# Kernel tuning notes

Measured on AMD Instinct MI355X. Metric: run time of the kernel, lower is better.

The kernel has to match this reference:

```python
import jax, jax.numpy as jnp
import numpy as np

N_QUBITS = 8
DEPTH = 2
INPUT_DIM = 64
HIDDEN_DIM = 8
SEQ_LEN = 128
BATCH = 512
DIM = 2 ** N_QUBITS


def _build_perm():
    """Compose the depth*n CNOT ring (CNOT(i,(i+1)%n) for i in range(n), repeated DEPTH times)
    into a single basis-state permutation. Wire 0 is the most-significant qubit (torchquantum order).
    CNOT is an involution on basis states: new[s] = old[f(s)], f flips target bit iff control bit set.
    Sequential composition: perm <- perm[f_j]."""
    n = N_QUBITS
    perm = np.arange(DIM)
    for _ in range(DEPTH):
        for c in range(n):
            t = (c + 1) % n
            s = np.arange(DIM)
            cbit = (s >> (n - 1 - c)) & 1
            fs = np.where(cbit == 1, s ^ (1 << (n - 1 - t)), s)
            perm = perm[fs]
    return jnp.asarray(perm, dtype=jnp.int32)


def _build_signs():
    s = np.arange(DIM)[:, None]
    w = np.arange(N_QUBITS)[None, :]
    bits = (s >> (N_QUBITS - 1 - w)) & 1
    return jnp.asarray(1.0 - 2.0 * bits, dtype=jnp.float32)  # [DIM, n]


PERM = _build_perm()
SIGNS = _build_signs()


def _qlayer(ang):
    """QLayer: RX(ang_i) on wire i of |0...0> (encoder RX + trainable RX fused since RX(a)RX(b)=RX(a+b)),
    then DEPTH CNOT-ring layers (precomputed permutation), then PauliZ expectation per wire.
    ang: [B, n] -> returns [B, n]."""
    half = 0.5 * ang
    v0 = jnp.cos(half).astype(jnp.complex64)          # [B, n]
    v1 = (-1j) * jnp.sin(half).astype(jnp.complex64)  # RX|0> = cos(t/2)|0> - i sin(t/2)|1>
    vecs = jnp.stack([v0, v1], axis=-1)               # [B, n, 2]
    b = ang.shape[0]
    state = jnp.ones((b, 1), jnp.complex64)
    for w in range(N_QUBITS):  # build product state, wire 0 most significant
        state = (state[:, :, None] * vecs[:, w, None, :]).reshape(b, -1)
    state = state[:, PERM]  # apply composed CNOT entanglers
    probs = jnp.real(state * jnp.conj(state)).astype(jnp.float32)  # [B, 2^n]
    return probs @ SIGNS  # [B, n] PauliZ expectations


def setup_inputs() -> dict:
    key = jax.random.key(0)
    ks = jax.random.split(key, 14)
    d = {"inputs": jax.random.normal(ks[0], (SEQ_LEN, BATCH, INPUT_DIM), jnp.float32)}
    fan_in = INPUT_DIM + HIDDEN_DIM
    scale = 1.0 / np.sqrt(fan_in)
    names = ["f", "i", "u", "o"]
    for j, nm in enumerate(names):
        d[f"W_{nm}"] = jax.random.uniform(ks[1 + 3 * j], (N_QUBITS, fan_in), jnp.float32, -scale, scale)
        d[f"b_{nm}"] = jax.random.uniform(ks[2 + 3 * j], (N_QUBITS,), jnp.float32, -scale, scale)
        d[f"th_{nm}"] = jax.random.normal(ks[3 + 3 * j], (N_QUBITS,), jnp.float32) * 0.1
    return d


def reference(inputs, W_f, b_f, W_i, b_i, W_u, b_u, W_o, b_o, th_f, th_i, th_u, th_o):
    batch = inputs.shape[1]

    def step(carry, x):
        hx, cx = carry
        comb = jnp.concatenate([x, hx], axis=1)  # [B, input+hidden]
        f = jax.nn.sigmoid(_qlayer(comb @ W_f.T + b_f + th_f))
        i = jax.nn.sigmoid(_qlayer(comb @ W_i.T + b_i + th_i))
        g = jnp.tanh(_qlayer(comb @ W_u.T + b_u + th_u))
        o = jax.nn.sigmoid(_qlayer(comb @ W_o.T + b_o + th_o))
        cx = f * cx + i * g
        hx = o * jnp.tanh(cx)
        return (hx, cx), hx

    init = (jnp.zeros((batch, HIDDEN_DIM), jnp.float32), jnp.zeros((batch, HIDDEN_DIM), jnp.float32))
    (hx, cx), outputs = jax.lax.scan(step, init, inputs)
    return (outputs, (hx, cx))
```

## Files before the change

### kernel.cpp

```cpp
#include <hip/hip_runtime.h>
#include <cstdint>
#include <cstddef>


constexpr int SEQ    = 128;
constexpr int NBATCH = 512;
constexpr int INDIM  = 64;
constexpr int FANIN  = 72;
constexpr long OUT_HX = (long)SEQ * NBATCH * 8;
constexpr long OUT_CX = OUT_HX + (long)NBATCH * 8;

#define SWZ(v, imm) __int_as_float(__builtin_amdgcn_ds_swizzle(__float_as_int(v), (imm)))

__device__ __forceinline__ float fast_cos(float ang) {
    const float rev = ang * 0.15915494309189535f;
    return __builtin_amdgcn_cosf(__builtin_amdgcn_fractf(rev));
}

template <int CTRL> __device__ __forceinline__ float DPPF(float x) {
    return __int_as_float(__builtin_amdgcn_update_dpp(
        0, __float_as_int(x), CTRL, 0xF, 0xF, false));
}

__device__ __forceinline__ float xlane32(float x, bool hiHalf) {
#if __has_builtin(__builtin_amdgcn_permlane32_swap)
    typedef unsigned uint2v __attribute__((ext_vector_type(2)));
    uint2v r = __builtin_amdgcn_permlane32_swap(
        __float_as_uint(x), __float_as_uint(x), false, false);
    return __uint_as_float(hiHalf ? r[0] : r[1]);
#else
    (void)hiHalf;
    return __shfl_xor(x, 32, 64);
#endif
}

__global__ __launch_bounds__(256) void xproj_kernel(
    const float* __restrict__ x,
    const float* __restrict__ Wf, const float* __restrict__ bf, const float* __restrict__ thf,
    const float* __restrict__ Wi, const float* __restrict__ bi, const float* __restrict__ thi,
    const float* __restrict__ Wu, const float* __restrict__ bu, const float* __restrict__ thu,
    const float* __restrict__ Wo, const float* __restrict__ bo, const float* __restrict__ tho,
    float* __restrict__ xp)
{
    __shared__ float lx[128 * 68];
    __shared__ float lbias[32];
    const int tid = threadIdx.x;
    const long rowBase = (long)blockIdx.x * 128;

    if (tid < 32) {
        const int g = tid >> 3, w = tid & 7;
        const float* bg = (g == 0) ? bf : (g == 1) ? bi : (g == 2) ? bu : bo;
        const float* tg = (g == 0) ? thf : (g == 1) ? thi : (g == 2) ? thu : tho;
        lbias[tid] = bg[w] + tg[w];
    }

    const float4* xin = reinterpret_cast<const float4*>(x + rowBase * INDIM);
#pragma unroll
    for (int i = 0; i < 8; ++i) {
        const int f   = i * 256 + tid;
        const int row = f >> 4;
        const int kq  = f & 15;
        *reinterpret_cast<float4*>(&lx[row * 68 + kq * 4]) = xin[f];
    }
    __syncthreads();

    const int og = tid & 3;
    const int q  = tid >> 2;
    const float* Wg = (og == 0) ? Wf : (og == 1) ? Wi : (og == 2) ? Wu : Wo;

    float acc[2][8];
#pragma unroll
    for (int r = 0; r < 2; ++r)
#pragma unroll
        for (int j = 0; j < 8; ++j) acc[r][j] = 0.f;

#pragma unroll
    for (int k4 = 0; k4 < 16; ++k4) {
        const float4 x0 = *reinterpret_cast<const float4*>(&lx[q * 68 + k4 * 4]);
        const float4 x1 = *reinterpret_cast<const float4*>(&lx[(q + 64) * 68 + k4 * 4]);
#pragma unroll
        for (int j = 0; j < 8; ++j) {
            const float4 wv = *reinterpret_cast<const float4*>(Wg + j * FANIN + k4 * 4);
            acc[0][j] = fmaf(x0.x, wv.x, acc[0][j]);
            acc[0][j] = fmaf(x0.y, wv.y, acc[0][j]);
            acc[0][j] = fmaf(x0.z, wv.z, acc[0][j]);
            acc[0][j] = fmaf(x0.w, wv.w, acc[0][j]);
            acc[1][j] = fmaf(x1.x, wv.x, acc[1][j]);
            acc[1][j] = fmaf(x1.y, wv.y, acc[1][j]);
            acc[1][j] = fmaf(x1.z, wv.z, acc[1][j]);
            acc[1][j] = fmaf(x1.w, wv.w, acc[1][j]);
        }
    }

#pragma unroll
    for (int r = 0; r < 2; ++r) {
        float4 o0, o1;
        o0.x = acc[r][0] + lbias[og * 8 + 0];
        o0.y = acc[r][1] + lbias[og * 8 + 1];
        o0.z = acc[r][2] + lbias[og * 8 + 2];
        o0.w = acc[r][3] + lbias[og * 8 + 3];
        o1.x = acc[r][4] + lbias[og * 8 + 4];
        o1.y = acc[r][5] + lbias[og * 8 + 5];
        o1.z = acc[r][6] + lbias[og * 8 + 6];
        o1.w = acc[r][7] + lbias[og * 8 + 7];
        float* dst = xp + (rowBase + q + 64 * r) * 32 + og * 8;
        reinterpret_cast<float4*>(dst)[0] = o0;
        reinterpret_cast<float4*>(dst)[1] = o1;
    }
}

__global__ __launch_bounds__(256) void qlstm_scan_kernel(
    const float* __restrict__ xp,
    const float* __restrict__ Wf, const float* __restrict__ Wi,
    const float* __restrict__ Wu, const float* __restrict__ Wo,
    float* __restrict__ out)
{
    const int tid  = threadIdx.x;
    const int lane = tid & 63;
    const int wv   = tid >> 6;
    const int g1   = (lane >> 5) & 1;
    const int g    = (lane & 1) | (g1 << 1);
    const int w    = (lane >> 1) & 7;
    const int rsub = (lane >> 4) & 1;
    const int row  = (blockIdx.x << 3) + (wv << 1) + rsub;

    const float* Wg = (g == 0) ? Wf : (g == 1) ? Wi : (g == 2) ? Wu : Wo;

    float whx[8];
#pragma unroll
    for (int d = 0; d < 8; ++d) whx[d] = Wg[w * FANIN + 64 + (w ^ d)];

    const unsigned mask = (unsigned)((0x55AAD5EAF5FAFDABull >> (w * 8)) & 0xFFull);
    bool pm[8];
#pragma unroll
    for (int d = 0; d < 8; ++d) pm[d] = ((mask >> (w ^ d)) & 1u) != 0u;

    const bool  isU   = (g == 2);
    const float ZL    = isU ? -2.0f : -1.0f;
    const float A     = isU ?  2.0f :  1.0f;
    const float B     = isU ? -1.0f :  0.0f;
    const bool  gOdd  = (lane & 1) != 0;
    const bool  gHi   = g1 != 0;
    const bool  doOut = (lane & 0x21) == 0;

    const int col = g * 8 + w;

    float hh0=0.f,hh1=0.f,hh2=0.f,hh3=0.f,hh4=0.f,hh5=0.f,hh6=0.f,hh7=0.f;
    float cxl = 0.f;

#define QSTEP(XV, T) do {                                                      \
    const float d0_ = fmaf(hh0, whx[0], fmaf(hh1, whx[1], fmaf(hh2, whx[2], hh3 * whx[3]))); \
    const float d1_ = fmaf(hh4, whx[4], fmaf(hh5, whx[5], fmaf(hh6, whx[6], hh7 * whx[7]))); \
    const float ang_ = (XV) + d0_ + d1_;                                       \
    const float c0_ = fast_cos(ang_);                                          \
    const float c1_ = DPPF<0x4E>(c0_);                                         \
    const float c2_ = DPPF<0x141>(DPPF<0x1B>(c0_));                            \
    const float c3_ = DPPF<0x141>(DPPF<0xB1>(c0_));                            \
    const float c4_ = DPPF<0x128>(c0_);                                        \
    const float c5_ = DPPF<0x128>(DPPF<0x4E>(c0_));                            \
    const float c6_ = DPPF<0x140>(DPPF<0x1B>(c0_));                            \
    const float c7_ = DPPF<0x140>(DPPF<0xB1>(c0_));                            \
    const float z_ = (((pm[0]?c0_:1.0f)*(pm[1]?c1_:1.0f))                      \
                    * ((pm[2]?c2_:1.0f)*(pm[3]?c3_:1.0f)))                     \
                   * (((pm[4]?c4_:1.0f)*(pm[5]?c5_:1.0f))                      \
                    * ((pm[6]?c6_:1.0f)*(pm[7]?c7_:1.0f)));                    \
    const float e_   = __expf(z_ * ZL);                                        \
    const float act_ = fmaf(A, __builtin_amdgcn_rcpf(1.0f + e_), B);           \
    const float a01_ = DPPF<0xB1>(act_);                                       \
    const float ae_  = gOdd ? a01_ : act_;                                     \
    const float ao_  = gOdd ? act_ : a01_;                                     \
    const float be_  = xlane32(ae_, gHi);                                      \
    const float bo_  = xlane32(ao_, gHi);                                      \
    const float fg_  = gHi ? be_ : ae_;                                        \
    const float ig_  = gHi ? bo_ : ao_;                                        \
    const float ug_  = gHi ? ae_ : be_;                                        \
    const float og_  = gHi ? ao_ : bo_;                                        \
    const float ncx_ = fmaf(fg_, cxl, ig_ * ug_);                              \
    const float et_  = __expf(-2.0f * ncx_);                                   \
    const float tc_  = fmaf(2.0f, __builtin_amdgcn_rcpf(1.0f + et_), -1.0f);   \
    const float nhx_ = og_ * tc_;                                              \
    cxl = ncx_;                                                                \
    if (doOut) out[((long)(T) * NBATCH + row) * 8 + w] = nhx_;                 \
    hh0 = nhx_;                                                                \
    hh1 = DPPF<0x4E>(nhx_);                                                    \
    hh2 = DPPF<0x141>(DPPF<0x1B>(nhx_));                                       \
    hh3 = DPPF<0x141>(DPPF<0xB1>(nhx_));                                       \
    hh4 = DPPF<0x128>(nhx_);                                                   \
    hh5 = DPPF<0x128>(DPPF<0x4E>(nhx_));                                       \
    hh6 = DPPF<0x140>(DPPF<0x1B>(nhx_));                                       \
    hh7 = DPPF<0x140>(DPPF<0xB1>(nhx_));                                       \
} while (0)

    float xva[16], xvb[16];
#pragma unroll
    for (int j = 0; j < 16; ++j)
        xva[j] = xp[((long)j * NBATCH + row) * 32 + col];

#pragma unroll 1
    for (int ck = 0; ck < 8; ++ck) {
        const int t0 = ck * 16;
        if (ck < 7) {
#pragma unroll
            for (int j = 0; j < 16; ++j)
                xvb[j] = xp[((long)(t0 + 16 + j) * NBATCH + row) * 32 + col];
        }
#pragma unroll
        for (int j = 0; j < 16; ++j) {
            QSTEP(xva[j], t0 + j);
        }
#pragma unroll
        for (int j = 0; j < 16; ++j) xva[j] = xvb[j];
    }
#undef QSTEP

    if (doOut) {
        out[OUT_HX + (long)row * 8 + w] = hh0;
        out[OUT_CX + (long)row * 8 + w] = cxl;
    }
}

__global__ __launch_bounds__(256) void qlstm_scan_fused(
    const float* __restrict__ x,
    const float* __restrict__ Wf, const float* __restrict__ bf, const float* __restrict__ thf,
    const float* __restrict__ Wi, const float* __restrict__ bi, const float* __restrict__ thi,
    const float* __restrict__ Wu, const float* __restrict__ bu, const float* __restrict__ thu,
    const float* __restrict__ Wo, const float* __restrict__ bo, const float* __restrict__ tho,
    float* __restrict__ out)
{
    const int tid  = threadIdx.x;
    const int lane = tid & 31;
    const int row  = (blockIdx.x << 3) + (tid >> 5);
    const int g    = lane >> 3;
    const int w    = lane & 7;

    const float* Wg = (g == 0) ? Wf : (g == 1) ? Wi : (g == 2) ? Wu : Wo;
    const float* bg = (g == 0) ? bf : (g == 1) ? bi : (g == 2) ? bu : bo;
    const float* tg = (g == 0) ? thf : (g == 1) ? thi : (g == 2) ? thu : tho;

    float wh0, wh1, wh2, wh3, wh4, wh5, wh6, wh7;
    {
        const float4* p = reinterpret_cast<const float4*>(Wg + w * FANIN + 64);
        const float4 a = p[0], b4 = p[1];
        wh0 = a.x; wh1 = a.y; wh2 = a.z; wh3 = a.w;
        wh4 = b4.x; wh5 = b4.y; wh6 = b4.z; wh7 = b4.w;
    }
    const float bias = bg[w] + tg[w];
    float wx[64];
#pragma unroll
    for (int k4 = 0; k4 < 16; ++k4) {
        const float4 v = reinterpret_cast<const float4*>(Wg + w * FANIN)[k4];
        wx[4*k4+0] = v.x; wx[4*k4+1] = v.y; wx[4*k4+2] = v.z; wx[4*k4+3] = v.w;
    }

    const unsigned mask = (unsigned)((0x55AAD5EAF5FAFDABull >> (w * 8)) & 0xFFull);
    const bool  isU = (g == 2);
    const float ZL  = isU ? -2.0f : -1.0f;
    const float A   = isU ?  2.0f :  1.0f;
    const float B   = isU ? -1.0f :  0.0f;

    float h0=0,h1=0,h2=0,h3=0,h4=0,h5=0,h6=0,h7=0, cxl=0, nhx=0;

    for (int t = 0; t < SEQ; ++t) {
        const float4* xr4 = reinterpret_cast<const float4*>(x + ((long)t * NBATCH + row) * INDIM);
        float acc = bias;
#pragma unroll
        for (int k4 = 0; k4 < 16; ++k4) {
            const float4 v = xr4[k4];
            acc = fmaf(v.x, wx[4*k4+0], acc);
            acc = fmaf(v.y, wx[4*k4+1], acc);
            acc = fmaf(v.z, wx[4*k4+2], acc);
            acc = fmaf(v.w, wx[4*k4+3], acc);
        }
        float ang = acc;
        ang += fmaf(h0, wh0, fmaf(h1, wh1, fmaf(h2, wh2, h3 * wh3)))
             + fmaf(h4, wh4, fmaf(h5, wh5, fmaf(h6, wh6, h7 * wh7)));

        const float c = fast_cos(ang);
        const float cb0 = SWZ(c, 0x018); const float cb1 = SWZ(c, 0x038);
        const float cb2 = SWZ(c, 0x058); const float cb3 = SWZ(c, 0x078);
        const float cb4 = SWZ(c, 0x098); const float cb5 = SWZ(c, 0x0B8);
        const float cb6 = SWZ(c, 0x0D8); const float cb7 = SWZ(c, 0x0F8);

        const float p0 = (mask & 0x01u) ? cb0 : 1.0f;
        const float p1 = (mask & 0x02u) ? cb1 : 1.0f;
        const float p2 = (mask & 0x04u) ? cb2 : 1.0f;
        const float p3 = (mask & 0x08u) ? cb3 : 1.0f;
        const float p4 = (mask & 0x10u) ? cb4 : 1.0f;
        const float p5 = (mask & 0x20u) ? cb5 : 1.0f;
        const float p6 = (mask & 0x40u) ? cb6 : 1.0f;
        const float p7 = (mask & 0x80u) ? cb7 : 1.0f;
        const float z = ((p0*p1)*(p2*p3)) * ((p4*p5)*(p6*p7));

        const float e   = __expf(z * ZL);
        const float act = fmaf(A, __builtin_amdgcn_rcpf(1.0f + e), B);

        const float fg = SWZ(act, 0x007);
        const float ig = SWZ(act, 0x107);
        const float ug = SWZ(act, 0x207);
        const float og = SWZ(act, 0x307);

        const float ncx = fmaf(fg, cxl, ig * ug);
        const float et  = __expf(-2.0f * ncx);
        const float tc  = fmaf(2.0f, __builtin_amdgcn_rcpf(1.0f + et), -1.0f);
        nhx = og * tc;
        cxl = ncx;

        if (lane < 8) out[((long)t * NBATCH + row) * 8 + lane] = nhx;

        h0 = SWZ(nhx, 0x000); h1 = SWZ(nhx, 0x020);
        h2 = SWZ(nhx, 0x040); h3 = SWZ(nhx, 0x060);
        h4 = SWZ(nhx, 0x080); h5 = SWZ(nhx, 0x0A0);
        h6 = SWZ(nhx, 0x0C0); h7 = SWZ(nhx, 0x0E0);
    }

    if (lane < 8) {
        out[OUT_HX + (long)row * 8 + lane] = nhx;
        out[OUT_CX + (long)row * 8 + lane] = cxl;
    }
}

extern "C" void kernel_launch(void* const* d_in, const int* in_sizes, int n_in,
                              void* d_out, int out_size, void* d_ws, size_t ws_size,
                              hipStream_t stream)
{
    const float* x = (const float*)d_in[0];

    const float *Wf, *bf, *thf, *Wi, *bi, *thi, *Wu, *bu, *thu, *Wo, *bo, *tho;
    if (in_sizes[3] == 8) {
        Wf = (const float*)d_in[1];  bf = (const float*)d_in[2];  thf = (const float*)d_in[3];
        Wi = (const float*)d_in[4];  bi = (const float*)d_in[5];  thi = (const float*)d_in[6];
        Wu = (const float*)d_in[7];  bu = (const float*)d_in[8];  thu = (const float*)d_in[9];
        Wo = (const float*)d_in[10]; bo = (const float*)d_in[11]; tho = (const float*)d_in[12];
    } else {
        Wf = (const float*)d_in[1];  bf = (const float*)d_in[2];
        Wi = (const float*)d_in[3];  bi = (const float*)d_in[4];
        Wu = (const float*)d_in[5];  bu = (const float*)d_in[6];
        Wo = (const float*)d_in[7];  bo = (const float*)d_in[8];
        thf = (const float*)d_in[9]; thi = (const float*)d_in[10];
        thu = (const float*)d_in[11]; tho = (const float*)d_in[12];
    }

    float* out = (float*)d_out;
    float* xp  = (float*)d_ws;
    const size_t need = (size_t)SEQ * NBATCH * 32 * sizeof(float);

    if (ws_size >= need) {
        xproj_kernel<<<(SEQ * NBATCH) / 128, 256, 0, stream>>>(
            x, Wf, bf, thf, Wi, bi, thi, Wu, bu, thu, Wo, bo, tho, xp);
        qlstm_scan_kernel<<<NBATCH / 8, 256, 0, stream>>>(
            xp, Wf, Wi, Wu, Wo, out);
    } else {
        qlstm_scan_fused<<<NBATCH / 8, 256, 0, stream>>>(
            x, Wf, bf, thf, Wi, bi, thi, Wu, bu, thu, Wo, bo, tho, out);
    }
}
```

Measured before the change: 148.7 us.

## Interleave two independent batch rows per thread in the scan kernel

Each thread now runs the recurrent step for two batch rows (row and row+256) in an interleaved fashion, halving the grid from 64 to 32 blocks. The goal is to hide the long serial dependency chain (cos, DPP shuffles, exp, rcp) of each timestep by giving the scheduler two independent chains per wave. The x-projection prefetch chunk shrinks from 16 to 8 steps per row to keep register use similar. The trade-off is fewer waves on the GPU and more registers per thread, which may cut latency hiding at the wave level.

```diff
diff --git a/kernel.cpp b/kernel.cpp
--- a/kernel.cpp
+++ b/kernel.cpp
@@ -109,6 +109,63 @@
     }
 }
 
+__device__ __forceinline__ void qstep(
+    float xv, int t, int row, int w,
+    const float whx[8], const bool pm[8],
+    float ZL, float A, float B, bool gOdd, bool gHi, bool doOut,
+    float& hh0, float& hh1, float& hh2, float& hh3,
+    float& hh4, float& hh5, float& hh6, float& hh7,
+    float& cxl, float* __restrict__ out)
+{
+    const float d0 = fmaf(hh0, whx[0], fmaf(hh1, whx[1], fmaf(hh2, whx[2], hh3 * whx[3])));
+    const float d1 = fmaf(hh4, whx[4], fmaf(hh5, whx[5], fmaf(hh6, whx[6], hh7 * whx[7])));
+    const float ang = xv + d0 + d1;
+
+    const float c0 = fast_cos(ang);
+    const float c1 = DPPF<0x4E>(c0);
+    const float c2 = DPPF<0x141>(DPPF<0x1B>(c0));
+    const float c3 = DPPF<0x141>(DPPF<0xB1>(c0));
+    const float c4 = DPPF<0x128>(c0);
+    const float c5 = DPPF<0x128>(DPPF<0x4E>(c0));
+    const float c6 = DPPF<0x140>(DPPF<0x1B>(c0));
+    const float c7 = DPPF<0x140>(DPPF<0xB1>(c0));
+
+    const float z = (((pm[0] ? c0 : 1.0f) * (pm[1] ? c1 : 1.0f))
+                   * ((pm[2] ? c2 : 1.0f) * (pm[3] ? c3 : 1.0f)))
+                  * (((pm[4] ? c4 : 1.0f) * (pm[5] ? c5 : 1.0f))
+                   * ((pm[6] ? c6 : 1.0f) * (pm[7] ? c7 : 1.0f)));
+
+    const float e   = __expf(z * ZL);
+    const float act = fmaf(A, __builtin_amdgcn_rcpf(1.0f + e), B);
+
+    const float a01 = DPPF<0xB1>(act);
+    const float ae  = gOdd ? a01 : act;
+    const float ao  = gOdd ? act : a01;
+    const float be  = xlane32(ae, gHi);
+    const float bo  = xlane32(ao, gHi);
+    const float fg  = gHi ? be : ae;
+    const float ig  = gHi ? bo : ao;
+    const float ug  = gHi ? ae : be;
+    const float og  = gHi ? ao : bo;
+
+    const float ncx = fmaf(fg, cxl, ig * ug);
+    const float et  = __expf(-2.0f * ncx);
+    const float tc  = fmaf(2.0f, __builtin_amdgcn_rcpf(1.0f + et), -1.0f);
+    const float nhx = og * tc;
+    cxl = ncx;
+
+    if (doOut) out[((long)t * NBATCH + row) * 8 + w] = nhx;
+
+    hh0 = nhx;
+    hh1 = DPPF<0x4E>(nhx);
+    hh2 = DPPF<0x141>(DPPF<0x1B>(nhx));
+    hh3 = DPPF<0x141>(DPPF<0xB1>(nhx));
+    hh4 = DPPF<0x128>(nhx);
+    hh5 = DPPF<0x128>(DPPF<0x4E>(nhx));
+    hh6 = DPPF<0x140>(DPPF<0x1B>(nhx));
+    hh7 = DPPF<0x140>(DPPF<0xB1>(nhx));
+}
+
 __global__ __launch_bounds__(256) void qlstm_scan_kernel(
     const float* __restrict__ xp,
     const float* __restrict__ Wf, const float* __restrict__ Wi,
@@ -122,7 +179,8 @@
     const int g    = (lane & 1) | (g1 << 1);
     const int w    = (lane >> 1) & 7;
     const int rsub = (lane >> 4) & 1;
-    const int row  = (blockIdx.x << 3) + (wv << 1) + rsub;
+    const int rowL = (blockIdx.x << 3) + (wv << 1) + rsub;
+    const int rowH = rowL + 256;
 
     const float* Wg = (g == 0) ? Wf : (g == 1) ? Wi : (g == 2) ? Wu : Wo;
 
@@ -145,77 +203,42 @@
 
     const int col = g * 8 + w;
 
-    float hh0=0.f,hh1=0.f,hh2=0.f,hh3=0.f,hh4=0.f,hh5=0.f,hh6=0.f,hh7=0.f;
-    float cxl = 0.f;
-
-#define QSTEP(XV, T) do {                                                      \
-    const float d0_ = fmaf(hh0, whx[0], fmaf(hh1, whx[1], fmaf(hh2, whx[2], hh3 * whx[3]))); \
-    const float d1_ = fmaf(hh4, whx[4], fmaf(hh5, whx[5], fmaf(hh6, whx[6], hh7 * whx[7]))); \
-    const float ang_ = (XV) + d0_ + d1_;                                       \
-    const float c0_ = fast_cos(ang_);                                          \
-    const float c1_ = DPPF<0x4E>(c0_);                                         \
-    const float c2_ = DPPF<0x141>(DPPF<0x1B>(c0_));                            \
-    const float c3_ = DPPF<0x141>(DPPF<0xB1>(c0_));                            \
-    const float c4_ = DPPF<0x128>(c0_);                                        \
-    const float c5_ = DPPF<0x128>(DPPF<0x4E>(c0_));                            \
-    const float c6_ = DPPF<0x140>(DPPF<0x1B>(c0_));                            \
-    const float c7_ = DPPF<0x140>(DPPF<0xB1>(c0_));                            \
-    const float z_ = (((pm[0]?c0_:1.0f)*(pm[1]?c1_:1.0f))                      \
-                    * ((pm[2]?c2_:1.0f)*(pm[3]?c3_:1.0f)))                     \
-                   * (((pm[4]?c4_:1.0f)*(pm[5]?c5_:1.0f))                      \
-                    * ((pm[6]?c6_:1.0f)*(pm[7]?c7_:1.0f)));                    \
-    const float e_   = __expf(z_ * ZL);                                        \
-    const float act_ = fmaf(A, __builtin_amdgcn_rcpf(1.0f + e_), B);           \
-    const float a01_ = DPPF<0xB1>(act_);                                       \
-    const float ae_  = gOdd ? a01_ : act_;                                     \
-    const float ao_  = gOdd ? act_ : a01_;                                     \
-    const float be_  = xlane32(ae_, gHi);                                      \
-    const float bo_  = xlane32(ao_, gHi);                                      \
-    const float fg_  = gHi ? be_ : ae_;                                        \
-    const float ig_  = gHi ? bo_ : ao_;                                        \
-    const float ug_  = gHi ? ae_ : be_;                                        \
-    const float og_  = gHi ? ao_ : bo_;                                        \
-    const float ncx_ = fmaf(fg_, cxl, ig_ * ug_);                              \
-    const float et_  = __expf(-2.0f * ncx_);                                   \
-    const float tc_  = fmaf(2.0f, __builtin_amdgcn_rcpf(1.0f + et_), -1.0f);   \
-    const float nhx_ = og_ * tc_;                                              \
-    cxl = ncx_;                                                                \
-    if (doOut) out[((long)(T) * NBATCH + row) * 8 + w] = nhx_;                 \
-    hh0 = nhx_;                                                                \
-    hh1 = DPPF<0x4E>(nhx_);                                                    \
-    hh2 = DPPF<0x141>(DPPF<0x1B>(nhx_));                                       \
-    hh3 = DPPF<0x141>(DPPF<0xB1>(nhx_));                                       \
-    hh4 = DPPF<0x128>(nhx_);                                                   \
-    hh5 = DPPF<0x128>(DPPF<0x4E>(nhx_));                                       \
-    hh6 = DPPF<0x140>(DPPF<0x1B>(nhx_));                                       \
-    hh7 = DPPF<0x140>(DPPF<0xB1>(nhx_));                                       \
-} while (0)
-
-    float xva[16], xvb[16];
-#pragma unroll
-    for (int j = 0; j < 16; ++j)
-        xva[j] = xp[((long)j * NBATCH + row) * 32 + col];
+    float hL0=0.f,hL1=0.f,hL2=0.f,hL3=0.f,hL4=0.f,hL5=0.f,hL6=0.f,hL7=0.f,cxL=0.f;
+    float hH0=0.f,hH1=0.f,hH2=0.f,hH3=0.f,hH4=0.f,hH5=0.f,hH6=0.f,hH7=0.f,cxH=0.f;
+
+    float xvaL[8], xvbL[8], xvaH[8], xvbH[8];
+#pragma unroll
+    for (int j = 0; j < 8; ++j) {
+        xvaL[j] = xp[((long)j * NBATCH + rowL) * 32 + col];
+        xvaH[j] = xp[((long)j * NBATCH + rowH) * 32 + col];
+    }
 
 #pragma unroll 1
-    for (int ck = 0; ck < 8; ++ck) {
-        const int t0 = ck * 16;
-        if (ck < 7) {
-#pragma unroll
-            for (int j = 0; j < 16; ++j)
-                xvb[j] = xp[((long)(t0 + 16 + j) * NBATCH + row) * 32 + col];
+    for (int ck = 0; ck < 16; ++ck) {
+        const int t0 = ck * 8;
+        if (ck < 15) {
+#pragma unroll
+            for (int j = 0; j < 8; ++j) {
+                xvbL[j] = xp[((long)(t0 + 8 + j) * NBATCH + rowL) * 32 + col];
+                xvbH[j] = xp[((long)(t0 + 8 + j) * NBATCH + rowH) * 32 + col];
+            }
         }
 #pragma unroll
-        for (int j = 0; j < 16; ++j) {
-            QSTEP(xva[j], t0 + j);
+        for (int j = 0; j < 8; ++j) {
+            qstep(xvaL[j], t0 + j, rowL, w, whx, pm, ZL, A, B, gOdd, gHi, doOut,
+                  hL0, hL1, hL2, hL3, hL4, hL5, hL6, hL7, cxL, out);
+            qstep(xvaH[j], t0 + j, rowH, w, whx, pm, ZL, A, B, gOdd, gHi, doOut,
+                  hH0, hH1, hH2, hH3, hH4, hH5, hH6, hH7, cxH, out);
         }
 #pragma unroll
-        for (int j = 0; j < 16; ++j) xva[j] = xvb[j];
-    }
-#undef QSTEP
+        for (int j = 0; j < 8; ++j) { xvaL[j] = xvbL[j]; xvaH[j] = xvbH[j]; }
+    }
 
     if (doOut) {
-        out[OUT_HX + (long)row * 8 + w] = hh0;
-        out[OUT_CX + (long)row * 8 + w] = cxl;
+        out[OUT_HX + (long)rowL * 8 + w] = hL0;
+        out[OUT_CX + (long)rowL * 8 + w] = cxL;
+        out[OUT_HX + (long)rowH * 8 + w] = hH0;
+        out[OUT_CX + (long)rowH * 8 + w] = cxH;
     }
 }
 
@@ -347,7 +370,7 @@
     if (ws_size >= need) {
         xproj_kernel<<<(SEQ * NBATCH) / 128, 256, 0, stream>>>(
             x, Wf, bf, thf, Wi, bi, thi, Wu, bu, thu, Wo, bo, tho, xp);
-        qlstm_scan_kernel<<<NBATCH / 8, 256, 0, stream>>>(
+        qlstm_scan_kernel<<<NBATCH / 16, 256, 0, stream>>>(
             xp, Wf, Wi, Wu, Wo, out);
     } else {
         qlstm_scan_fused<<<NBATCH / 8, 256, 0, stream>>>(
```

After: 176.4 us. 18.6% more time.
